# Optimization experiments

Hardware: AMD Instinct MI355X
Metric: run time of the kernel (lower is better)

## Reference

```python
import jax, jax.numpy as jnp
import numpy as np

IMAGE_SIZE = 224
COV_HP = 1.0
SIGMA = 1.0
STEPS = 2
CUTOFF = 20.0
IMP_LO, IMP_HI = 0.5, 2.0
REL_W = 0.5
EPS = 1e-6

# Projection matrices for front/top/left views (buffer Js in the module)
JS = jnp.array([[[1, 0, 0], [0, 1, 0]],
                [[1, 0, 0], [0, 0, 1]],
                [[0, 0, 1], [0, 1, 0]]], dtype=jnp.float32)


def _blur(d, sigma):
    # d: [B,H,W]; separable Gaussian blur, 'same' padding
    r = max(1, int(3 * sigma))
    x = jnp.arange(-r, r + 1, dtype=jnp.float32)
    k = jnp.exp(-(x * x) / (2.0 * sigma * sigma))
    k = k / k.sum()
    d4 = d[:, None]  # [B,1,H,W]
    kh = k.reshape(1, 1, -1, 1)
    kw = k.reshape(1, 1, 1, -1)
    d4 = jax.lax.conv_general_dilated(d4, kh, (1, 1), [(r, r), (0, 0)],
                                      dimension_numbers=('NCHW', 'OIHW', 'NCHW'))
    d4 = jax.lax.conv_general_dilated(d4, kw, (1, 1), [(0, 0), (r, r)],
                                      dimension_numbers=('NCHW', 'OIHW', 'NCHW'))
    return d4[:, 0]


def _fill_depth_map(d, sigma, steps):
    # fill_depth_map is not defined in the source; implemented as iterative
    # Gaussian-blur hole filling (empty pixels take blurred neighborhood).
    for _ in range(steps):
        b = _blur(d, sigma)
        d = jnp.where(d > 1e-6, d, b)
    return d


def _forward(position, cov3d, opacity, importance):
    B, N, _ = position.shape
    H = W = IMAGE_SIZE
    Hh, Wh = H // 2, W // 2
    yy, xx = jnp.meshgrid(jnp.arange(Hh), jnp.arange(Wh), indexing='ij')
    grid = jnp.stack([xx, yy], axis=-1).astype(jnp.float32)  # [Hh,Wh,2]
    imp = jnp.clip(jnp.broadcast_to(importance[:, :N], (B, N)), IMP_LO, IMP_HI)
    imp = imp[:, :, None, None]
    eye3 = jnp.eye(3, dtype=cov3d.dtype)
    eye2 = jnp.eye(2, dtype=cov3d.dtype)
    maps = []
    for v in range(3):  # fixed small view loop, as in the source
        J = JS[v]  # [2,3]
        # NOTE: source mutates cov3d across the view loop; replicate that
        cov3d = (cov3d + jnp.swapaxes(cov3d, -1, -2)) * 0.5
        cov3d = cov3d + EPS * eye3
        nrm = jnp.linalg.norm(cov3d, axis=(-1, -2), keepdims=True)
        cov3d = cov3d / (nrm + EPS) * COV_HP
        cinv = jnp.linalg.inv(cov3d)                               # [B,N,3,3]
        cov2d_inv = jnp.einsum('ij,bnjk,lk->bnil', J, cinv, J)     # J C^-1 J^T
        cov2d_inv = cov2d_inv + eye2 * (EPS * 1e-4)
        proj = jnp.einsum('bnk,jk->bnj', position, J)              # [B,N,2]
        mn = proj.min(axis=1, keepdims=True)
        mx = proj.max(axis=1, keepdims=True)
        rng = mx - mn + 1e-6
        mn = mn - 0.5 * rng
        mx = mx + 0.5 * rng
        rng = mx - mn + 1e-6
        xy = jnp.clip((proj - mn) / rng * (Wh - 1), 0.0, Wh - 1)
        delta = grid[None, None] - xy[:, :, None, None, :]         # [B,N,Hh,Wh,2]
        mask_h = jnp.linalg.norm(delta, axis=-1) < CUTOFF
        mask = jnp.repeat(jnp.repeat(mask_h, 2, axis=2), 2, axis=3)
        exph = -jnp.einsum('bnhwj,bnjk,bnhwk->bnhw', delta, cov2d_inv, delta)
        exp_full = jax.image.resize(exph, (B, N, H, W), method='bilinear')
        exp_full = jnp.clip(exp_full, -20.0, 0.0)
        w = opacity[:, :, None, None] * imp * jnp.exp(exp_full)
        w = jnp.where(mask, w, 0.0)
        wmin = w.min(axis=1, keepdims=True)
        wmax = w.max(axis=1, keepdims=True)
        nw = (w - wmin) / (wmax - wmin + EPS) * REL_W + w / (w.sum(axis=1, keepdims=True) + EPS)
        dm = nw.sum(axis=1)  # [B,H,W]
        maps.append(_fill_depth_map(dm, SIGMA, STEPS))
    d = jnp.stack(maps, axis=1)  # [B,3,H,W], already 224x224 so resize is a no-op
    d = (d - d.mean()) / (jnp.std(d, ddof=1) + EPS)
    return d


def setup_inputs() -> dict:
    key = jax.random.key(0)
    k1, k2, k3 = jax.random.split(key, 3)
    B, N, MAXG = 1, 512, 1000
    return {
        'position': jax.random.normal(k1, (B, N, 3), dtype=jnp.float32),
        'cov3d': jax.random.normal(k2, (B, N, 3, 3), dtype=jnp.float32),
        'opacity': jax.random.uniform(k3, (B, N), dtype=jnp.float32),
        'importance': jnp.ones((1, MAXG), dtype=jnp.float32),
    }


def reference(position, cov3d, opacity, importance):
    return _forward(position, cov3d, opacity, importance)
```

## Files before the change

### kernel.cpp

```cpp
#include <hip/hip_runtime.h>
#include <math.h>


#define NBLOCKS 588u
#define NARR 32
#define FLAG_IDX (NARR * 32)

__device__ __forceinline__ float g_ld(const float* p) {
    return __hip_atomic_load(p, __ATOMIC_RELAXED, __HIP_MEMORY_SCOPE_AGENT);
}
__device__ __forceinline__ void g_st(float* p, float v) {
    __hip_atomic_store(p, v, __ATOMIC_RELAXED, __HIP_MEMORY_SCOPE_AGENT);
}

__device__ __forceinline__ void grid_barrier(unsigned* cnts, int arrIdx, bool poller) {
    __syncthreads();
    if (threadIdx.x == 0) {
        asm volatile("s_waitcnt vmcnt(0)" ::: "memory");
        __hip_atomic_fetch_add(&cnts[arrIdx * 32], 1u,
                               __ATOMIC_RELAXED, __HIP_MEMORY_SCOPE_AGENT);
        unsigned* flagp = &cnts[FLAG_IDX];
        if (poller) {
            for (;;) {
                unsigned s = 0;
                #pragma unroll
                for (int i = 0; i < NARR; ++i)
                    s += __hip_atomic_load(&cnts[i * 32],
                                           __ATOMIC_RELAXED, __HIP_MEMORY_SCOPE_AGENT);
                if (s == NBLOCKS) break;
                __builtin_amdgcn_s_sleep(2);
            }
            asm volatile("" ::: "memory");
            __hip_atomic_store(flagp, 1u, __ATOMIC_RELAXED, __HIP_MEMORY_SCOPE_AGENT);
        } else {
            while (__hip_atomic_load(flagp, __ATOMIC_RELAXED,
                                     __HIP_MEMORY_SCOPE_AGENT) == 0u)
                __builtin_amdgcn_s_sleep(2);
        }
    }
    __syncthreads();
}

__device__ __forceinline__ float wave_min(float v) {
    #pragma unroll
    for (int o = 32; o >= 1; o >>= 1) v = fminf(v, __shfl_xor(v, o));
    return v;
}

__global__ __launch_bounds__(512) void splat_fused_kernel(
    const float* __restrict__ position, const float* __restrict__ cov3d,
    const float* __restrict__ opacity, const float* __restrict__ importance,
    float* __restrict__ dm, unsigned* __restrict__ cnts) {
    __shared__ float4 lsA[512];
    __shared__ float2 lsB[512];
    __shared__ float red[8 * 6];
    __shared__ float4 pS[7][64], pMn[7][64], pMx[7][64];
    __shared__ int cnt;
    const int v = blockIdx.z;
    const int tx0 = blockIdx.x * 16, ty0 = blockIdx.y * 16;
    const int tid = threadIdx.x;
    const int lane = tid & 63, wave = tid >> 6;

    if (blockIdx.x == 0 && blockIdx.y == 0 && blockIdx.z == 0) {
        for (int i = tid; i <= FLAG_IDX; i += 512) cnts[i] = 0;
    }

    const int n = tid;
    const float p0 = position[n * 3 + 0];
    const float p1 = position[n * 3 + 1];
    const float p2 = position[n * 3 + 2];
    const float opimp = opacity[n] * fminf(fmaxf(importance[n], 0.5f), 2.0f);

    {
        float vals[6] = {p0, -p0, p1, -p1, p2, -p2};
        #pragma unroll
        for (int k = 0; k < 6; ++k) {
            float r = wave_min(vals[k]);
            if (lane == 0) red[wave * 6 + k] = r;
        }
    }
    __syncthreads();
    float mn6[6];
    #pragma unroll
    for (int k = 0; k < 6; ++k) {
        float r = red[k];
        #pragma unroll
        for (int w = 1; w < 8; ++w) r = fminf(r, red[w * 6 + k]);
        mn6[k] = r;
    }
    const float pmn[3] = {mn6[0], mn6[2], mn6[4]};
    const float pmx[3] = {-mn6[1], -mn6[3], -mn6[5]};

    float c00 = cov3d[n * 9 + 0], c01 = cov3d[n * 9 + 1], c02 = cov3d[n * 9 + 2];
    float c10 = cov3d[n * 9 + 3], c11 = cov3d[n * 9 + 4], c12 = cov3d[n * 9 + 5];
    float c20 = cov3d[n * 9 + 6], c21 = cov3d[n * 9 + 7], c22 = cov3d[n * 9 + 8];
    for (int vv = 0; vv <= v; ++vv) {
        float s01 = 0.5f * (c01 + c10);
        float s02 = 0.5f * (c02 + c20);
        float s12 = 0.5f * (c12 + c21);
        float s00 = c00 + 1e-6f;
        float s11 = c11 + 1e-6f;
        float s22 = c22 + 1e-6f;
        float nrm = sqrtf(s00 * s00 + s11 * s11 + s22 * s22 +
                          2.0f * (s01 * s01 + s02 * s02 + s12 * s12));
        float inv = 1.0f / (nrm + 1e-6f);
        c00 = s00 * inv; c11 = s11 * inv; c22 = s22 * inv;
        c01 = s01 * inv; c10 = c01; c02 = s02 * inv; c20 = c02;
        c12 = s12 * inv; c21 = c12;
    }
    float cof00 = c11 * c22 - c12 * c12;
    float cof01 = c02 * c12 - c01 * c22;
    float cof02 = c01 * c12 - c02 * c11;
    float det = c00 * cof00 + c01 * cof01 + c02 * cof02;
    float idet = 1.0f / det;
    float i00 = cof00 * idet;
    float i01 = cof01 * idet;
    float i02 = cof02 * idet;
    float i11 = (c00 * c22 - c02 * c02) * idet;
    float i12 = (c02 * c01 - c00 * c12) * idet;
    float i22 = (c00 * c11 - c01 * c01) * idet;

    float Aa, Ab, Ac, prx, pry;
    int ix, iy;
    if (v == 0)      { Aa = i00; Ab = i01; Ac = i11; prx = p0; pry = p1; ix = 0; iy = 1; }
    else if (v == 1) { Aa = i00; Ab = i02; Ac = i22; prx = p0; pry = p2; ix = 0; iy = 2; }
    else             { Aa = i22; Ab = i12; Ac = i11; prx = p2; pry = p1; ix = 2; iy = 1; }
    Aa += 1e-10f;
    Ac += 1e-10f;

    float mnx = pmn[ix], mxx = pmx[ix], mny = pmn[iy], mxy = pmx[iy];
    float rngx = mxx - mnx + 1e-6f;
    float mnx2 = mnx - 0.5f * rngx;
    float mxx2 = mxx + 0.5f * rngx;
    rngx = mxx2 - mnx2 + 1e-6f;
    float rngy = mxy - mny + 1e-6f;
    float mny2 = mny - 0.5f * rngy;
    float mxy2 = mxy + 0.5f * rngy;
    rngy = mxy2 - mny2 + 1e-6f;
    float gx = fminf(fmaxf((prx - mnx2) / rngx * 111.0f, 0.0f), 111.0f);
    float gy = fminf(fmaxf((pry - mny2) / rngy * 111.0f, 0.0f), 111.0f);

    if (tid == 0) cnt = 0;
    __syncthreads();
    {
        const float bx0 = (float)(tx0 >> 1), bx1 = (float)((tx0 + 15) >> 1);
        const float by0 = (float)(ty0 >> 1), by1 = (float)((ty0 + 15) >> 1);
        float dx = fmaxf(fmaxf(bx0 - gx, gx - bx1), 0.0f);
        float dy = fmaxf(fmaxf(by0 - gy, gy - by1), 0.0f);
        bool pass = (dx * dx + dy * dy) < 400.01f;
        unsigned long long m = __ballot(pass);
        int base = 0;
        if (lane == 0) base = atomicAdd(&cnt, __popcll(m));
        base = __shfl(base, 0);
        if (pass) {
            int slot = base + __popcll(m & ((1ull << lane) - 1ull));
            lsA[slot] = make_float4(Aa, 2.0f * Ab, Ac, opimp);
            lsB[slot] = make_float2(gx, gy);
        }
    }
    __syncthreads();
    const int len = cnt;

    const int qx = lane & 7, qy = lane >> 3;
    const int xh = (tx0 >> 1) + qx;
    const int yh = (ty0 >> 1) + qy;

    if (len == 0) {
        if (wave == 0) {
            #pragma unroll
            for (int py = 0; py < 2; ++py)
                #pragma unroll
                for (int px = 0; px < 2; ++px)
                    dm[(v * 224 + ty0 + 2 * qy + py) * 224 + tx0 + 2 * qx + px] = 0.0f;
        }
        return;
    }

    const int npad = (len + 15) & ~15;
    if (tid < npad - len) {
        lsA[len + tid] = make_float4(1.0f, 0.0f, 1.0f, 0.0f);
        lsB[len + tid] = make_float2(1e9f, 1e9f);
    }
    __syncthreads();

    float exA[2], eyA[2], VxA[2], VyA[2];
    #pragma unroll
    for (int p = 0; p < 2; ++p) {
        int xlo = xh - 1 + p; int xhi = min(xlo + 1, 111); xlo = max(xlo, 0);
        float wlo = p ? 0.75f : 0.25f, whi = 1.0f - wlo;
        exA[p] = wlo * (float)xlo + whi * (float)xhi;
        VxA[p] = wlo * whi * (float)(xhi - xlo) * (float)(xhi - xlo);
        int ylo = yh - 1 + p; int yhi2 = min(ylo + 1, 111); ylo = max(ylo, 0);
        eyA[p] = wlo * (float)ylo + whi * (float)yhi2;
        VyA[p] = wlo * whi * (float)(yhi2 - ylo) * (float)(yhi2 - ylo);
    }
    const float fxh = (float)xh, fyh = (float)yh;

    const int chunk = npad >> 3;
    const int cbeg = wave * chunk, cend = cbeg + chunk;

    float S00 = 0.f, S01 = 0.f, S10 = 0.f, S11 = 0.f;
    float mn00 = INFINITY, mn01 = INFINITY, mn10 = INFINITY, mn11 = INFINITY;
    float mx00 = -INFINITY, mx01 = -INFINITY, mx10 = -INFINITY, mx11 = -INFINITY;

    for (int i = cbeg; i < cend; i += 2) {
        float4 gA0 = lsA[i], gA1 = lsA[i + 1];
        float2 gB0 = lsB[i], gB1 = lsB[i + 1];
        #pragma unroll
        for (int u = 0; u < 2; ++u) {
            const float4 gA = u ? gA1 : gA0;
            const float2 gB = u ? gB1 : gB0;
            const float a = gA.x, b2 = gA.y, c = gA.z, op = gA.w;
            const float xx = gB.x, yy = gB.y;
            const float dxh = fxh - xx, dyh = fyh - yy;
            const bool inside = dxh * dxh + dyh * dyh < 400.0f;
            const float dx0 = exA[0] - xx, dx1 = exA[1] - xx;
            const float dy0 = eyA[0] - yy, dy1 = eyA[1] - yy;
            const float adx0 = a * dx0, adx1 = a * dx1;
            const float bdy0 = b2 * dy0, bdy1 = b2 * dy1;
            const float cdy0 = c * dy0 * dy0, cdy1 = c * dy1 * dy1;
            const float ax0 = a * VxA[0], ax1 = a * VxA[1];
            const float cy0 = c * VyA[0], cy1 = c * VyA[1];
            #pragma unroll
            for (int py = 0; py < 2; ++py) {
                const float bdyp = py ? bdy1 : bdy0;
                const float cdyp = py ? cdy1 : cdy0;
                const float cyp  = py ? cy1 : cy0;
                #pragma unroll
                for (int px = 0; px < 2; ++px) {
                    const float dxp  = px ? dx1 : dx0;
                    const float adxp = px ? adx1 : adx0;
                    const float axp  = px ? ax1 : ax0;
                    float q = dxp * (adxp + bdyp) + cdyp;
                    float bil = -((q + axp) + cyp);
                    bil = fminf(fmaxf(bil, -20.0f), 0.0f);
                    bil = inside ? bil : -1e9f;
                    float w = op * __expf(bil);
                    if (py == 0 && px == 0) { S00 += w; mn00 = fminf(mn00, w); mx00 = fmaxf(mx00, w); }
                    if (py == 0 && px == 1) { S01 += w; mn01 = fminf(mn01, w); mx01 = fmaxf(mx01, w); }
                    if (py == 1 && px == 0) { S10 += w; mn10 = fminf(mn10, w); mx10 = fmaxf(mx10, w); }
                    if (py == 1 && px == 1) { S11 += w; mn11 = fminf(mn11, w); mx11 = fmaxf(mx11, w); }
                }
            }
        }
    }
    if (wave > 0) {
        pS[wave - 1][lane]  = make_float4(S00, S01, S10, S11);
        pMn[wave - 1][lane] = make_float4(mn00, mn01, mn10, mn11);
        pMx[wave - 1][lane] = make_float4(mx00, mx01, mx10, mx11);
    }
    __syncthreads();
    if (wave == 0) {
        #pragma unroll
        for (int k = 0; k < 7; ++k) {
            float4 s = pS[k][lane], m = pMn[k][lane], M = pMx[k][lane];
            S00 += s.x; S01 += s.y; S10 += s.z; S11 += s.w;
            mn00 = fminf(mn00, m.x); mn01 = fminf(mn01, m.y);
            mn10 = fminf(mn10, m.z); mn11 = fminf(mn11, m.w);
            mx00 = fmaxf(mx00, M.x); mx01 = fmaxf(mx01, M.y);
            mx10 = fmaxf(mx10, M.z); mx11 = fmaxf(mx11, M.w);
        }
        if (len < 512) {
            mn00 = fminf(mn00, 0.f); mn01 = fminf(mn01, 0.f);
            mn10 = fminf(mn10, 0.f); mn11 = fminf(mn11, 0.f);
            mx00 = fmaxf(mx00, 0.f); mx01 = fmaxf(mx01, 0.f);
            mx11 = fmaxf(mx11, 0.f); mx10 = fmaxf(mx10, 0.f);
        }
        float S4[4]  = {S00, S01, S10, S11};
        float mn4[4] = {mn00, mn01, mn10, mn11};
        float mx4[4] = {mx00, mx01, mx10, mx11};
        #pragma unroll
        for (int pp = 0; pp < 4; ++pp) {
            float S = S4[pp];
            float dmv = 0.5f * (S - 512.0f * mn4[pp]) / (mx4[pp] - mn4[pp] + 1e-6f)
                      + S / (S + 1e-6f);
            const int py = pp >> 1, px = pp & 1;
            dm[(v * 224 + ty0 + 2 * qy + py) * 224 + tx0 + 2 * qx + px] = dmv;
        }
    }
}

__global__ __launch_bounds__(256, 3) void blur_norm_kernel(
    const float* __restrict__ in, float* __restrict__ out,
    float2* __restrict__ partials, unsigned* __restrict__ cnts) {
    __shared__ float A[28 * 29];
    __shared__ float T[28 * 29];
    __shared__ float r1[4], r2[4];
    __shared__ double s1[256], s2[256];
    const int v = blockIdx.z;
    const int tx0 = blockIdx.x * 16, ty0 = blockIdx.y * 16;
    const int tid = threadIdx.x;
    const int lane = tid & 63, wave = tid >> 6;
    const int bid = (v * 14 + blockIdx.y) * 14 + blockIdx.x;
    const float kw[7] = {0.00443305f, 0.05400558f, 0.24203623f, 0.39905030f,
                         0.24203623f, 0.05400558f, 0.00443305f};
    const float* __restrict__ chan = in + v * 224 * 224;

    for (int idx = tid; idx < 28 * 28; idx += 256) {
        int rr = idx / 28, c = idx % 28;
        int gyy = ty0 - 6 + rr, gxx = tx0 - 6 + c;
        float val = 0.0f;
        if (gyy >= 0 && gyy < 224 && gxx >= 0 && gxx < 224) val = chan[gyy * 224 + gxx];
        A[rr * 29 + c] = val;
    }
    __syncthreads();
    for (int idx = tid; idx < 22 * 28; idx += 256) {
        int rr = 3 + idx / 28, c = idx % 28;
        float s = 0.0f;
        #pragma unroll
        for (int i = 0; i < 7; ++i) s += kw[i] * A[(rr - 3 + i) * 29 + c];
        T[rr * 29 + c] = s;
    }
    __syncthreads();
    for (int idx = tid; idx < 22 * 22; idx += 256) {
        int rr = 3 + idx / 22, c = 3 + idx % 22;
        int gyy = ty0 - 6 + rr, gxx = tx0 - 6 + c;
        float s = 0.0f;
        #pragma unroll
        for (int j = 0; j < 7; ++j) s += kw[j] * T[rr * 29 + c - 3 + j];
        float ctr = A[rr * 29 + c];
        float d1 = ctr > 1e-6f ? ctr : s;
        if (gyy < 0 || gyy > 223 || gxx < 0 || gxx > 223) d1 = 0.0f;
        A[rr * 29 + c] = d1;
    }
    __syncthreads();
    for (int idx = tid; idx < 16 * 22; idx += 256) {
        int rr = 6 + idx / 22, c = 3 + idx % 22;
        float s = 0.0f;
        #pragma unroll
        for (int i = 0; i < 7; ++i) s += kw[i] * A[(rr - 3 + i) * 29 + c];
        T[rr * 29 + c] = s;
    }
    __syncthreads();
    const int rr2 = 6 + (tid >> 4), cc2 = 6 + (tid & 15);
    float d2;
    {
        float s = 0.0f;
        #pragma unroll
        for (int j = 0; j < 7; ++j) s += kw[j] * T[rr2 * 29 + cc2 - 3 + j];
        float ctr = A[rr2 * 29 + cc2];
        d2 = ctr > 1e-6f ? ctr : s;
    }
    float ls1 = d2, ls2 = d2 * d2;
    #pragma unroll
    for (int o = 32; o >= 1; o >>= 1) {
        ls1 += __shfl_xor(ls1, o);
        ls2 += __shfl_xor(ls2, o);
    }
    if (lane == 0) { r1[wave] = ls1; r2[wave] = ls2; }
    __syncthreads();
    if (tid == 0) {
        float a = r1[0] + r1[1] + r1[2] + r1[3];
        float b = r2[0] + r2[1] + r2[2] + r2[3];
        float* pb = (float*)&partials[bid];
        g_st(pb + 0, a);
        g_st(pb + 1, b);
    }

    grid_barrier(cnts, bid & (NARR - 1), bid == 0);

    double a = 0.0, b = 0.0;
    const float* pb = (const float*)partials;
    for (int i = tid; i < 588; i += 256) {
        a += (double)g_ld(pb + 2 * i);
        b += (double)g_ld(pb + 2 * i + 1);
    }
    s1[tid] = a; s2[tid] = b;
    __syncthreads();
    for (int s = 128; s >= 1; s >>= 1) {
        if (tid < s) { s1[tid] += s1[tid + s]; s2[tid] += s2[tid + s]; }
        __syncthreads();
    }
    const double M = 150528.0;
    double mean = s1[0] / M;
    double var = (s2[0] - M * mean * mean) / (M - 1.0);
    double sd = sqrt(var > 0.0 ? var : 0.0);
    const float fmean = (float)mean;
    const float finv = 1.0f / ((float)sd + 1e-6f);
    out[(v * 224 + ty0 + (tid >> 4)) * 224 + tx0 + (tid & 15)] =
        (d2 - fmean) * finv;
}

extern "C" void kernel_launch(void* const* d_in, const int* in_sizes, int n_in,
                              void* d_out, int out_size, void* d_ws, size_t ws_size,
                              hipStream_t stream) {
    const float* position   = (const float*)d_in[0];
    const float* cov3d      = (const float*)d_in[1];
    const float* opacity    = (const float*)d_in[2];
    const float* importance = (const float*)d_in[3];
    float* out = (float*)d_out;

    float* dmA       = (float*)d_ws;
    float2* partials = (float2*)((float*)d_ws + 150528);
    unsigned* cnts   = (unsigned*)((float*)d_ws + 150528 + 1176);

    hipLaunchKernelGGL(splat_fused_kernel, dim3(14, 14, 3), dim3(512), 0, stream,
                       position, cov3d, opacity, importance, dmA, cnts);
    hipLaunchKernelGGL(blur_norm_kernel, dim3(14, 14, 3), dim3(256), 0, stream,
                       dmA, out, partials, cnts);
}
```

Before: 90.01 us.

## Split splat gaussian loop across four blocks and merge partials in blur kernel

The splat kernel now launches four times as many blocks, and each one processes a quarter of the padded, culled gaussian list for its tile. Each block writes per-pixel partial sums, minima and maxima to a 12-float workspace record. The blur kernel's load stage merges these partials and computes the depth value before blurring. This adds parallelism to the per-tile work so more CUs stay busy. In exchange, every block repeats the setup work (covariance recursion, culling, compaction), the workspace writes and reads grow substantially, and the early exit for empty tiles is gone. Compaction also moves from a shared atomic counter to a per-wave count prefix.

```diff
diff --git a/kernel.cpp b/kernel.cpp
--- a/kernel.cpp
+++ b/kernel.cpp
@@ -5,6 +5,7 @@
 #define NBLOCKS 588u
 #define NARR 32
 #define FLAG_IDX (NARR * 32)
+#define KSPLIT 4
 
 __device__ __forceinline__ float g_ld(const float* p) {
     return __hip_atomic_load(p, __ATOMIC_RELAXED, __HIP_MEMORY_SCOPE_AGENT);
@@ -47,16 +48,17 @@
     return v;
 }
 
-__global__ __launch_bounds__(512) void splat_fused_kernel(
+__global__ __launch_bounds__(512) void splat_part_kernel(
     const float* __restrict__ position, const float* __restrict__ cov3d,
     const float* __restrict__ opacity, const float* __restrict__ importance,
-    float* __restrict__ dm, unsigned* __restrict__ cnts) {
+    float* __restrict__ part, unsigned* __restrict__ cnts) {
     __shared__ float4 lsA[512];
     __shared__ float2 lsB[512];
     __shared__ float red[8 * 6];
+    __shared__ int wcnt[8];
     __shared__ float4 pS[7][64], pMn[7][64], pMx[7][64];
-    __shared__ int cnt;
-    const int v = blockIdx.z;
+    const int v  = blockIdx.z >> 2;
+    const int kk = blockIdx.z & 3;
     const int tx0 = blockIdx.x * 16, ty0 = blockIdx.y * 16;
     const int tid = threadIdx.x;
     const int lane = tid & 63, wave = tid >> 6;
@@ -74,19 +76,19 @@
     {
         float vals[6] = {p0, -p0, p1, -p1, p2, -p2};
         #pragma unroll
-        for (int k = 0; k < 6; ++k) {
-            float r = wave_min(vals[k]);
-            if (lane == 0) red[wave * 6 + k] = r;
+        for (int q = 0; q < 6; ++q) {
+            float r = wave_min(vals[q]);
+            if (lane == 0) red[wave * 6 + q] = r;
         }
     }
     __syncthreads();
     float mn6[6];
     #pragma unroll
-    for (int k = 0; k < 6; ++k) {
-        float r = red[k];
-        #pragma unroll
-        for (int w = 1; w < 8; ++w) r = fminf(r, red[w * 6 + k]);
-        mn6[k] = r;
+    for (int q = 0; q < 6; ++q) {
+        float r = red[q];
+        #pragma unroll
+        for (int w = 1; w < 8; ++w) r = fminf(r, red[w * 6 + q]);
+        mn6[q] = r;
     }
     const float pmn[3] = {mn6[0], mn6[2], mn6[4]};
     const float pmx[3] = {-mn6[1], -mn6[3], -mn6[5]};
@@ -140,43 +142,38 @@
     float gx = fminf(fmaxf((prx - mnx2) / rngx * 111.0f, 0.0f), 111.0f);
     float gy = fminf(fmaxf((pry - mny2) / rngy * 111.0f, 0.0f), 111.0f);
 
-    if (tid == 0) cnt = 0;
-    __syncthreads();
+    unsigned long long m;
+    bool pass;
     {
         const float bx0 = (float)(tx0 >> 1), bx1 = (float)((tx0 + 15) >> 1);
         const float by0 = (float)(ty0 >> 1), by1 = (float)((ty0 + 15) >> 1);
         float dx = fmaxf(fmaxf(bx0 - gx, gx - bx1), 0.0f);
         float dy = fmaxf(fmaxf(by0 - gy, gy - by1), 0.0f);
-        bool pass = (dx * dx + dy * dy) < 400.01f;
-        unsigned long long m = __ballot(pass);
-        int base = 0;
-        if (lane == 0) base = atomicAdd(&cnt, __popcll(m));
-        base = __shfl(base, 0);
-        if (pass) {
-            int slot = base + __popcll(m & ((1ull << lane) - 1ull));
-            lsA[slot] = make_float4(Aa, 2.0f * Ab, Ac, opimp);
-            lsB[slot] = make_float2(gx, gy);
-        }
-    }
-    __syncthreads();
-    const int len = cnt;
+        pass = (dx * dx + dy * dy) < 400.01f;
+        m = __ballot(pass);
+        if (lane == 0) wcnt[wave] = __popcll(m);
+    }
+    __syncthreads();
+    int base = 0, lentot = 0;
+    #pragma unroll
+    for (int w = 0; w < 8; ++w) {
+        int c = wcnt[w];
+        if (w < wave) base += c;
+        lentot += c;
+    }
+    if (pass) {
+        int slot = base + __popcll(m & ((1ull << lane) - 1ull));
+        lsA[slot] = make_float4(Aa, 2.0f * Ab, Ac, opimp);
+        lsB[slot] = make_float2(gx, gy);
+    }
+    __syncthreads();
+    const int len = lentot;
 
     const int qx = lane & 7, qy = lane >> 3;
     const int xh = (tx0 >> 1) + qx;
     const int yh = (ty0 >> 1) + qy;
 
-    if (len == 0) {
-        if (wave == 0) {
-            #pragma unroll
-            for (int py = 0; py < 2; ++py)
-                #pragma unroll
-                for (int px = 0; px < 2; ++px)
-                    dm[(v * 224 + ty0 + 2 * qy + py) * 224 + tx0 + 2 * qx + px] = 0.0f;
-        }
-        return;
-    }
-
-    const int npad = (len + 15) & ~15;
+    const int npad = (len + 63) & ~63;
     if (tid < npad - len) {
         lsA[len + tid] = make_float4(1.0f, 0.0f, 1.0f, 0.0f);
         lsB[len + tid] = make_float2(1e9f, 1e9f);
@@ -196,8 +193,8 @@
     }
     const float fxh = (float)xh, fyh = (float)yh;
 
-    const int chunk = npad >> 3;
-    const int cbeg = wave * chunk, cend = cbeg + chunk;
+    const int chunk = npad >> 5;
+    const int cbeg = ((kk << 3) + wave) * chunk, cend = cbeg + chunk;
 
     float S00 = 0.f, S01 = 0.f, S10 = 0.f, S11 = 0.f;
     float mn00 = INFINITY, mn01 = INFINITY, mn10 = INFINITY, mn11 = INFINITY;
@@ -252,36 +249,37 @@
     __syncthreads();
     if (wave == 0) {
         #pragma unroll
-        for (int k = 0; k < 7; ++k) {
-            float4 s = pS[k][lane], m = pMn[k][lane], M = pMx[k][lane];
+        for (int w = 0; w < 7; ++w) {
+            float4 s = pS[w][lane], mnw = pMn[w][lane], mxw = pMx[w][lane];
             S00 += s.x; S01 += s.y; S10 += s.z; S11 += s.w;
-            mn00 = fminf(mn00, m.x); mn01 = fminf(mn01, m.y);
-            mn10 = fminf(mn10, m.z); mn11 = fminf(mn11, m.w);
-            mx00 = fmaxf(mx00, M.x); mx01 = fmaxf(mx01, M.y);
-            mx10 = fmaxf(mx10, M.z); mx11 = fmaxf(mx11, M.w);
+            mn00 = fminf(mn00, mnw.x); mn01 = fminf(mn01, mnw.y);
+            mn10 = fminf(mn10, mnw.z); mn11 = fminf(mn11, mnw.w);
+            mx00 = fmaxf(mx00, mxw.x); mx01 = fmaxf(mx01, mxw.y);
+            mx10 = fmaxf(mx10, mxw.z); mx11 = fmaxf(mx11, mxw.w);
         }
         if (len < 512) {
             mn00 = fminf(mn00, 0.f); mn01 = fminf(mn01, 0.f);
             mn10 = fminf(mn10, 0.f); mn11 = fminf(mn11, 0.f);
             mx00 = fmaxf(mx00, 0.f); mx01 = fmaxf(mx01, 0.f);
-            mx11 = fmaxf(mx11, 0.f); mx10 = fmaxf(mx10, 0.f);
+            mx10 = fmaxf(mx10, 0.f); mx11 = fmaxf(mx11, 0.f);
         }
         float S4[4]  = {S00, S01, S10, S11};
         float mn4[4] = {mn00, mn01, mn10, mn11};
         float mx4[4] = {mx00, mx01, mx10, mx11};
         #pragma unroll
         for (int pp = 0; pp < 4; ++pp) {
-            float S = S4[pp];
-            float dmv = 0.5f * (S - 512.0f * mn4[pp]) / (mx4[pp] - mn4[pp] + 1e-6f)
-                      + S / (S + 1e-6f);
             const int py = pp >> 1, px = pp & 1;
-            dm[(v * 224 + ty0 + 2 * qy + py) * 224 + tx0 + 2 * qx + px] = dmv;
+            const int y = ty0 + 2 * qy + py, x = tx0 + 2 * qx + px;
+            float* pb = part + ((v * 224 + y) * 224 + x) * 12 + kk;
+            pb[0] = S4[pp];
+            pb[4] = mn4[pp];
+            pb[8] = mx4[pp];
         }
     }
 }
 
 __global__ __launch_bounds__(256, 3) void blur_norm_kernel(
-    const float* __restrict__ in, float* __restrict__ out,
+    const float* __restrict__ part, float* __restrict__ out,
     float2* __restrict__ partials, unsigned* __restrict__ cnts) {
     __shared__ float A[28 * 29];
     __shared__ float T[28 * 29];
@@ -294,13 +292,21 @@
     const int bid = (v * 14 + blockIdx.y) * 14 + blockIdx.x;
     const float kw[7] = {0.00443305f, 0.05400558f, 0.24203623f, 0.39905030f,
                          0.24203623f, 0.05400558f, 0.00443305f};
-    const float* __restrict__ chan = in + v * 224 * 224;
 
     for (int idx = tid; idx < 28 * 28; idx += 256) {
         int rr = idx / 28, c = idx % 28;
         int gyy = ty0 - 6 + rr, gxx = tx0 - 6 + c;
         float val = 0.0f;
-        if (gyy >= 0 && gyy < 224 && gxx >= 0 && gxx < 224) val = chan[gyy * 224 + gxx];
+        if (gyy >= 0 && gyy < 224 && gxx >= 0 && gxx < 224) {
+            const float* pb = part + ((v * 224 + gyy) * 224 + gxx) * 12;
+            const float4 Sv  = *(const float4*)(pb);
+            const float4 mnv = *(const float4*)(pb + 4);
+            const float4 mxv = *(const float4*)(pb + 8);
+            float S  = (Sv.x + Sv.y) + (Sv.z + Sv.w);
+            float mn = fminf(fminf(mnv.x, mnv.y), fminf(mnv.z, mnv.w));
+            float mx = fmaxf(fmaxf(mxv.x, mxv.y), fmaxf(mxv.z, mxv.w));
+            val = 0.5f * (S - 512.0f * mn) / (mx - mn + 1e-6f) + S / (S + 1e-6f);
+        }
         A[rr * 29 + c] = val;
     }
     __syncthreads();
@@ -390,12 +396,12 @@
     const float* importance = (const float*)d_in[3];
     float* out = (float*)d_out;
 
-    float* dmA       = (float*)d_ws;
-    float2* partials = (float2*)((float*)d_ws + 150528);
-    unsigned* cnts   = (unsigned*)((float*)d_ws + 150528 + 1176);
-
-    hipLaunchKernelGGL(splat_fused_kernel, dim3(14, 14, 3), dim3(512), 0, stream,
-                       position, cov3d, opacity, importance, dmA, cnts);
+    float* part      = (float*)d_ws;
+    float2* partials = (float2*)((float*)d_ws + 1806336);
+    unsigned* cnts   = (unsigned*)((float*)d_ws + 1806336 + 1176);
+
+    hipLaunchKernelGGL(splat_part_kernel, dim3(14, 14, 3 * KSPLIT), dim3(512), 0,
+                       stream, position, cov3d, opacity, importance, part, cnts);
     hipLaunchKernelGGL(blur_norm_kernel, dim3(14, 14, 3), dim3(256), 0, stream,
-                       dmA, out, partials, cnts);
-}
+                       part, out, partials, cnts);
+}
```

After: 108.8 us. 1.21x slower.
